# Optimization experiments

Measured on AMD Instinct MI355X. Metric: run time of the kernel, lower is better.

## Reference

```python
import jax, jax.numpy as jnp
import numpy as np

SIZES = {"a": 1024, "b": 512, "c": 2048}
OUT = 1024
N_STREAMS = 3
EPS = 1e-5


def _layer_norm(x, w, b):
    mu = jnp.mean(x, axis=-1, keepdims=True)
    var = jnp.mean(jnp.square(x - mu), axis=-1, keepdims=True)
    return (x - mu) * jax.lax.rsqrt(var + EPS) * w + b


def setup_inputs() -> dict:
    key = jax.random.key(0)
    ks = iter(jax.random.split(key, 32))
    B = 32768
    inp = {}
    for name, d in SIZES.items():
        inp[f"x_{name}"] = jax.random.normal(next(ks), (B, d), dtype=jnp.float32)
        inp[f"ln_w_{name}"] = jnp.ones((d,), dtype=jnp.float32)
        inp[f"ln_b_{name}"] = jnp.zeros((d,), dtype=jnp.float32)
        inp[f"W_{name}"] = jax.random.normal(next(ks), (d, OUT), dtype=jnp.float32) / np.sqrt(d)
        inp[f"b_{name}"] = jnp.zeros((OUT,), dtype=jnp.float32)
        # gating linear: size -> n_streams * gate_size (gate_size = OUT, pointwise)
        inp[f"Wg_{name}"] = 0.005 * jax.random.normal(next(ks), (d, N_STREAMS * OUT), dtype=jnp.float32)
        inp[f"bg_{name}"] = jnp.zeros((N_STREAMS * OUT,), dtype=jnp.float32)
    return inp


def reference(x_a, ln_w_a, ln_b_a, W_a, b_a, Wg_a, bg_a,
              x_b, ln_w_b, ln_b_b, W_b, b_b, Wg_b, bg_b,
              x_c, ln_w_c, ln_b_c, W_c, b_c, Wg_c, bg_c):
    xs = [x_a, x_b, x_c]
    lns = [(ln_w_a, ln_b_a), (ln_w_b, ln_b_b), (ln_w_c, ln_b_c)]
    lins = [(W_a, b_a), (W_b, b_b), (W_c, b_c)]
    gats = [(Wg_a, bg_a), (Wg_b, bg_b), (Wg_c, bg_c)]

    gate_logits = 0.0
    outputs = []
    for x, (lw, lb), (W, b), (Wg, bg) in zip(xs, lns, lins, gats):
        f = jax.nn.relu(_layer_norm(x, lw, lb))          # [B, d]
        outputs.append(f @ W + b)                         # [B, OUT]
        gate_logits = gate_logits + (f @ Wg + bg)         # [B, 3*OUT]

    B = x_a.shape[0]
    gate = jax.nn.softmax(gate_logits.reshape(B, N_STREAMS, OUT), axis=1)  # [B,3,OUT]
    out = sum(gate[:, i] * outputs[i] for i in range(N_STREAMS))
    return out
```

## Files before the change

kernel.cpp:

```cpp
#include <hip/hip_runtime.h>
#include <hip/hip_bf16.h>
#include <stdint.h>

#define B_ROWS 32768
#define KTOT   3584
#define NC     6144
#define OUT_N  1024

typedef unsigned short ushort_t;
typedef __attribute__((ext_vector_type(8))) short bf16x8;
typedef __attribute__((ext_vector_type(4))) float f32x4;

__device__ __forceinline__ float b2f(unsigned short u) {
    union { unsigned int i; float f; } x; x.i = ((unsigned int)u) << 16; return x.f;
}
__device__ __forceinline__ unsigned short f2b(float f) {
    union { float f; unsigned int i; } x; x.f = f;
    unsigned int r = x.i + 0x7fffu + ((x.i >> 16) & 1u);
    return (unsigned short)(r >> 16);
}

__device__ __forceinline__ void gload_lds16(const void* g, void* l) {
    auto g1 = reinterpret_cast<const __attribute__((address_space(1))) char*>(
        reinterpret_cast<uintptr_t>(g));
    auto l3 = reinterpret_cast<__attribute__((address_space(3))) char*>(
        (uint32_t)reinterpret_cast<uintptr_t>(l));
    __builtin_amdgcn_global_load_lds(g1, l3, 16, 0, 0);
}

__global__ __launch_bounds__(256) void pack_wt_kernel(
    const float* __restrict__ Wa, const float* __restrict__ Wga,
    const float* __restrict__ Wb, const float* __restrict__ Wgb,
    const float* __restrict__ Wc, const float* __restrict__ Wgc,
    ushort_t* __restrict__ WT)
{
    int s = blockIdx.y;
    const float *Ws, *Wgs; int d, koff;
    if (s == 0)      { Ws = Wa; Wgs = Wga; d = 1024; koff = 0;    }
    else if (s == 1) { Ws = Wb; Wgs = Wgb; d = 512;  koff = 1024; }
    else             { Ws = Wc; Wgs = Wgc; d = 2048; koff = 1536; }
    int kt = blockIdx.x >> 6;
    int ntile = blockIdx.x & 63;
    if (kt >= (d >> 6)) return;
    int k0 = kt * 64, n0 = ntile * 64;
    const float* src; int ld, ncol0;
    if (n0 < 1024) { src = Ws;  ld = 1024; ncol0 = n0; }
    else           { src = Wgs; ld = 3072; ncol0 = n0 - 1024; }

    __shared__ float tile[64][65];
    int tx = threadIdx.x & 63, ty = threadIdx.x >> 6;
    for (int r = ty; r < 64; r += 4)
        tile[r][tx] = src[(size_t)(k0 + r) * ld + ncol0 + tx];
    __syncthreads();
    for (int r = ty; r < 64; r += 4)
        WT[(size_t)(n0 + r) * KTOT + koff + k0 + tx] = f2b(tile[tx][r]);
}

__global__ __launch_bounds__(256) void pack_bias_kernel(
    const float* __restrict__ ba, const float* __restrict__ bb, const float* __restrict__ bc,
    const float* __restrict__ bga, const float* __restrict__ bgb, const float* __restrict__ bgc,
    float* __restrict__ bias)
{
    int i = blockIdx.x * 256 + threadIdx.x;
    if (i >= NC) return;
    float v;
    if (i < 1024)      v = ba[i];
    else if (i < 2048) v = bb[i - 1024];
    else if (i < 3072) v = bc[i - 2048];
    else { int g = i - 3072; v = bga[g] + bgb[g] + bgc[g]; }
    bias[i] = v;
}

__global__ __launch_bounds__(256) void ln_relu_kernel(
    const float* __restrict__ xa, const float* __restrict__ xb, const float* __restrict__ xc,
    const float* __restrict__ wa, const float* __restrict__ wb, const float* __restrict__ wc,
    const float* __restrict__ ba, const float* __restrict__ bb, const float* __restrict__ bc,
    ushort_t* __restrict__ F)
{
    int row = blockIdx.x;
    int s = blockIdx.y;
    const float *x, *w, *b; int d, koff;
    if (s == 0)      { x = xa; w = wa; b = ba; d = 1024; koff = 0;    }
    else if (s == 1) { x = xb; w = wb; b = bb; d = 512;  koff = 1024; }
    else             { x = xc; w = wc; b = bc; d = 2048; koff = 1536; }
    const float* xr = x + (size_t)row * d;
    int tid = threadIdx.x;

    float s1 = 0.f, s2 = 0.f;
    for (int i = tid * 4; i < d; i += 1024) {
        float4 v = *(const float4*)(xr + i);
        s1 += v.x + v.y + v.z + v.w;
        s2 += v.x * v.x + v.y * v.y + v.z * v.z + v.w * v.w;
    }
    for (int o = 32; o > 0; o >>= 1) {
        s1 += __shfl_down(s1, o, 64);
        s2 += __shfl_down(s2, o, 64);
    }
    __shared__ float red1[4], red2[4], bcast[2];
    int wv = tid >> 6, ln = tid & 63;
    if (ln == 0) { red1[wv] = s1; red2[wv] = s2; }
    __syncthreads();
    if (tid == 0) {
        float t1 = red1[0] + red1[1] + red1[2] + red1[3];
        float t2 = red2[0] + red2[1] + red2[2] + red2[3];
        float mean = t1 / d;
        float var = t2 / d - mean * mean;
        bcast[0] = mean;
        bcast[1] = rsqrtf(var + 1e-5f);
    }
    __syncthreads();
    float mean = bcast[0], rstd = bcast[1];

    ushort_t* Fr = F + (size_t)row * KTOT + koff;
    for (int i = tid * 4; i < d; i += 1024) {
        float4 v  = *(const float4*)(xr + i);
        float4 wv4 = *(const float4*)(w + i);
        float4 bv4 = *(const float4*)(b + i);
        float o0 = fmaxf(0.f, (v.x - mean) * rstd * wv4.x + bv4.x);
        float o1 = fmaxf(0.f, (v.y - mean) * rstd * wv4.y + bv4.y);
        float o2 = fmaxf(0.f, (v.z - mean) * rstd * wv4.z + bv4.z);
        float o3 = fmaxf(0.f, (v.w - mean) * rstd * wv4.w + bv4.w);
        union { ushort_t u[4]; uint2 v2; } pk;
        pk.u[0] = f2b(o0); pk.u[1] = f2b(o1); pk.u[2] = f2b(o2); pk.u[3] = f2b(o3);
        *(uint2*)(Fr + i) = pk.v2;
    }
}

__global__ __launch_bounds__(512, 2) void gemm_kernel(
    const ushort_t* __restrict__ F, const ushort_t* __restrict__ WT,
    const float* __restrict__ bias, ushort_t* __restrict__ C)
{
    extern __shared__ ushort_t lds_u16[];
    char* lds = (char*)lds_u16;

    int bid = blockIdx.x;
    int newid = (bid & 7) * 384 + (bid >> 3);
    int rowpanel = newid / 24;
    int j = newid % 24;
    int row0 = rowpanel * 256;
    int n0, koff, klen, c0;
    if (j < 4)       { n0 = j * 256;            koff = 0;    klen = 1024; c0 = j * 256; }
    else if (j < 8)  { n0 = (j - 4) * 256;      koff = 1024; klen = 512;  c0 = 1024 + (j - 4) * 256; }
    else if (j < 12) { n0 = (j - 8) * 256;      koff = 1536; klen = 2048; c0 = 2048 + (j - 8) * 256; }
    else             { n0 = 1024 + (j - 12) * 256; koff = 0; klen = 3584; c0 = 3072 + (j - 12) * 256; }

    int tid = threadIdx.x, w = tid >> 6, l = tid & 63;
    int wm0 = (w >> 2) * 128;
    int wn0 = (w & 3) * 64;

    int srow = w * 32 + (l >> 3);
    int scol = (((l & 7) ^ (l >> 3)) << 3);
    const ushort_t* Ag = F  + (size_t)(row0 + srow) * KTOT + koff + scol;
    const ushort_t* Bg = WT + (size_t)(n0   + srow) * KTOT + koff + scol;
    char* ldsAw = lds + (size_t)w * 4096;

#define STAGE(bufsel, kt) do {                                              \
        const ushort_t* ag_ = Ag + (kt) * 64;                               \
        const ushort_t* bg_ = Bg + (kt) * 64;                               \
        char* la_ = ldsAw + (bufsel) * 65536;                               \
        _Pragma("unroll")                                                   \
        for (int jj = 0; jj < 4; ++jj) {                                    \
            gload_lds16(ag_ + jj * 8 * KTOT, la_ + jj * 1024);              \
            gload_lds16(bg_ + jj * 8 * KTOT, la_ + 32768 + jj * 1024);      \
        }                                                                   \
    } while (0)

    int rl = l & 15;
    int c16_0 = ((l >> 4)    ) ^ (l & 7);
    int c16_1 = ((l >> 4) + 4) ^ (l & 7);
    int aoff0 = (wm0 + rl) * 128 + c16_0 * 16;
    int aoff1 = (wm0 + rl) * 128 + c16_1 * 16;
    int boff0 = 32768 + (wn0 + rl) * 128 + c16_0 * 16;
    int boff1 = 32768 + (wn0 + rl) * 128 + c16_1 * 16;

    f32x4 acc[8][4];
    #pragma unroll
    for (int mi = 0; mi < 8; ++mi)
        #pragma unroll
        for (int ni = 0; ni < 4; ++ni)
            acc[mi][ni] = (f32x4){0.f, 0.f, 0.f, 0.f};

    int nkt = klen >> 6;

    STAGE(0, 0);
    STAGE(1, 1);

#define TILE_BODY(CUR, VMCNT_ASM, DO_STAGE, TNEXT)                          \
    {                                                                       \
        asm volatile(VMCNT_ASM ::: "memory");                               \
        __builtin_amdgcn_s_barrier();                                       \
        const char* Ab_ = lds + (CUR) * 65536;                              \
        bf16x8 a0[8], a1[8], b0[4], b1[4];                                  \
        _Pragma("unroll")                                                   \
        for (int mi = 0; mi < 8; ++mi)                                      \
            a0[mi] = *(const bf16x8*)(Ab_ + aoff0 + mi * 2048);             \
        _Pragma("unroll")                                                   \
        for (int ni = 0; ni < 4; ++ni)                                      \
            b0[ni] = *(const bf16x8*)(Ab_ + boff0 + ni * 2048);             \
        _Pragma("unroll")                                                   \
        for (int mi = 0; mi < 8; ++mi)                                      \
            a1[mi] = *(const bf16x8*)(Ab_ + aoff1 + mi * 2048);             \
        _Pragma("unroll")                                                   \
        for (int ni = 0; ni < 4; ++ni)                                      \
            b1[ni] = *(const bf16x8*)(Ab_ + boff1 + ni * 2048);             \
        __builtin_amdgcn_s_setprio(1);                                      \
        _Pragma("unroll")                                                   \
        for (int mi = 0; mi < 8; ++mi)                                      \
            _Pragma("unroll")                                               \
            for (int ni = 0; ni < 4; ++ni)                                  \
                acc[mi][ni] = __builtin_amdgcn_mfma_f32_16x16x32_bf16(      \
                    a0[mi], b0[ni], acc[mi][ni], 0, 0, 0);                  \
        __builtin_amdgcn_s_setprio(0);                                      \
        asm volatile("s_waitcnt lgkmcnt(0)" ::: "memory");                  \
        __builtin_amdgcn_s_barrier();                                       \
        if (DO_STAGE) STAGE(CUR, TNEXT);                                    \
        __builtin_amdgcn_s_setprio(1);                                      \
        _Pragma("unroll")                                                   \
        for (int mi = 0; mi < 8; ++mi)                                      \
            _Pragma("unroll")                                               \
            for (int ni = 0; ni < 4; ++ni)                                  \
                acc[mi][ni] = __builtin_amdgcn_mfma_f32_16x16x32_bf16(      \
                    a1[mi], b1[ni], acc[mi][ni], 0, 0, 0);                  \
        __builtin_amdgcn_s_setprio(0);                                      \
    }

    for (int t = 0; t < nkt - 1; ++t) {
        int cur = t & 1;
        TILE_BODY(cur, "s_waitcnt vmcnt(8)", (t + 2 < nkt), t + 2)
    }
    {
        int cur = (nkt - 1) & 1;
        TILE_BODY(cur, "s_waitcnt vmcnt(0)", false, 0)
    }
#undef TILE_BODY
#undef STAGE

    #pragma unroll
    for (int ni = 0; ni < 4; ++ni) {
        int col = c0 + wn0 + ni * 16 + rl;
        float bv = bias[col];
        #pragma unroll
        for (int mi = 0; mi < 8; ++mi) {
            int rbase = row0 + wm0 + mi * 16 + (l >> 4) * 4;
            #pragma unroll
            for (int r = 0; r < 4; ++r)
                C[(size_t)(rbase + r) * NC + col] = f2b(acc[mi][ni][r] + bv);
        }
    }
}

typedef __attribute__((ext_vector_type(8))) unsigned short u16x8;

__global__ __launch_bounds__(256) void fuse_kernel(
    const ushort_t* __restrict__ C, float* __restrict__ out)
{
    int t = blockIdx.x * 256 + threadIdx.x;
    int b  = t >> 7;
    int j0 = (t & 127) << 3;
    const ushort_t* Cr = C + (size_t)b * NC;
    u16x8 oa = *(const u16x8*)(Cr + j0);
    u16x8 ob = *(const u16x8*)(Cr + 1024 + j0);
    u16x8 oc = *(const u16x8*)(Cr + 2048 + j0);
    u16x8 g0 = *(const u16x8*)(Cr + 3072 + j0);
    u16x8 g1 = *(const u16x8*)(Cr + 4096 + j0);
    u16x8 g2 = *(const u16x8*)(Cr + 5120 + j0);
    float res[8];
    #pragma unroll
    for (int k = 0; k < 8; ++k) {
        float a0 = b2f(g0[k]), a1 = b2f(g1[k]), a2 = b2f(g2[k]);
        float m = fmaxf(a0, fmaxf(a1, a2));
        float e0 = __expf(a0 - m), e1 = __expf(a1 - m), e2 = __expf(a2 - m);
        float inv = 1.f / (e0 + e1 + e2);
        res[k] = (e0 * b2f(oa[k]) + e1 * b2f(ob[k]) + e2 * b2f(oc[k])) * inv;
    }
    float* op = out + (size_t)b * 1024 + j0;
    *(float4*)op       = (float4){res[0], res[1], res[2], res[3]};
    *(float4*)(op + 4) = (float4){res[4], res[5], res[6], res[7]};
}

extern "C" void kernel_launch(void* const* d_in, const int* in_sizes, int n_in,
                              void* d_out, int out_size, void* d_ws, size_t ws_size,
                              hipStream_t stream)
{
    const float* x_a   = (const float*)d_in[0];
    const float* lnw_a = (const float*)d_in[1];
    const float* lnb_a = (const float*)d_in[2];
    const float* W_a   = (const float*)d_in[3];
    const float* b_a   = (const float*)d_in[4];
    const float* Wg_a  = (const float*)d_in[5];
    const float* bg_a  = (const float*)d_in[6];
    const float* x_b   = (const float*)d_in[7];
    const float* lnw_b = (const float*)d_in[8];
    const float* lnb_b = (const float*)d_in[9];
    const float* W_b   = (const float*)d_in[10];
    const float* b_b   = (const float*)d_in[11];
    const float* Wg_b  = (const float*)d_in[12];
    const float* bg_b  = (const float*)d_in[13];
    const float* x_c   = (const float*)d_in[14];
    const float* lnw_c = (const float*)d_in[15];
    const float* lnb_c = (const float*)d_in[16];
    const float* W_c   = (const float*)d_in[17];
    const float* b_c   = (const float*)d_in[18];
    const float* Wg_c  = (const float*)d_in[19];
    const float* bg_c  = (const float*)d_in[20];

    char* ws = (char*)d_ws;
    ushort_t* F    = (ushort_t*)ws;
    ushort_t* WT   = (ushort_t*)(ws + 234881024);
    ushort_t* Cbuf = (ushort_t*)(ws + 234881024 + 29360128);
    float*    bias = (float*)   (ws + 234881024 + 29360128 + 402653184);

    hipLaunchKernelGGL(pack_wt_kernel, dim3(2048, 3), dim3(256), 0, stream,
                       W_a, Wg_a, W_b, Wg_b, W_c, Wg_c, WT);
    hipLaunchKernelGGL(pack_bias_kernel, dim3(24), dim3(256), 0, stream,
                       b_a, b_b, b_c, bg_a, bg_b, bg_c, bias);
    hipLaunchKernelGGL(ln_relu_kernel, dim3(32768, 3), dim3(256), 0, stream,
                       x_a, x_b, x_c, lnw_a, lnw_b, lnw_c, lnb_a, lnb_b, lnb_c, F);
    hipLaunchKernelGGL(gemm_kernel, dim3(3072), dim3(512), 131072, stream,
                       F, WT, bias, Cbuf);
    hipLaunchKernelGGL(fuse_kernel, dim3(16384), dim3(256), 0, stream,
                       Cbuf, (float*)d_out);
}
```

Before: 1.099 ms.

## Restructure GEMM main loop into four interleaved quadrant phases with staggered loads

Splits each K-tile of the bf16 GEMM into four MFMA quadrants. LDS reads and global-to-LDS staging for the next tiles are interleaved between them, so memory traffic overlaps compute at a finer grain. LDS reads use inline-asm ds_read_b128 with immediate offsets, and sched_barriers pin the order. The cost is more s_barriers per tile, and the loop clamps tail tile indices, so redundant loads are issued at the end.

```diff
diff --git a/kernel.cpp b/kernel.cpp
--- a/kernel.cpp
+++ b/kernel.cpp
@@ -26,6 +26,13 @@
     auto l3 = reinterpret_cast<__attribute__((address_space(3))) char*>(
         (uint32_t)reinterpret_cast<uintptr_t>(l));
     __builtin_amdgcn_global_load_lds(g1, l3, 16, 0, 0);
+}
+
+template<int OFF>
+__device__ __forceinline__ bf16x8 dsr(uint32_t addr) {
+    bf16x8 d;
+    asm volatile("ds_read_b128 %0, %1 offset:%2" : "=v"(d) : "v"(addr), "i"(OFF));
+    return d;
 }
 
 __global__ __launch_bounds__(256) void pack_wt_kernel(
@@ -131,7 +138,6 @@
     const float* __restrict__ bias, ushort_t* __restrict__ C)
 {
     extern __shared__ ushort_t lds_u16[];
-    char* lds = (char*)lds_u16;
 
     int bid = blockIdx.x;
     int newid = (bid & 7) * 384 + (bid >> 3);
@@ -152,26 +158,52 @@
     int scol = (((l & 7) ^ (l >> 3)) << 3);
     const ushort_t* Ag = F  + (size_t)(row0 + srow) * KTOT + koff + scol;
     const ushort_t* Bg = WT + (size_t)(n0   + srow) * KTOT + koff + scol;
-    char* ldsAw = lds + (size_t)w * 4096;
-
-#define STAGE(bufsel, kt) do {                                              \
-        const ushort_t* ag_ = Ag + (kt) * 64;                               \
-        const ushort_t* bg_ = Bg + (kt) * 64;                               \
-        char* la_ = ldsAw + (bufsel) * 65536;                               \
-        _Pragma("unroll")                                                   \
-        for (int jj = 0; jj < 4; ++jj) {                                    \
-            gload_lds16(ag_ + jj * 8 * KTOT, la_ + jj * 1024);              \
-            gload_lds16(bg_ + jj * 8 * KTOT, la_ + 32768 + jj * 1024);      \
-        }                                                                   \
-    } while (0)
+
+    uint32_t lds_base = (uint32_t)(uintptr_t)lds_u16;
+    uint32_t ldsStA = lds_base + (uint32_t)w * 4096u;
+
+#define STG_A(SELOFF, kt, JJ0) do {                                              \
+        gload_lds16(Ag + (size_t)(kt) * 64 + (size_t)(JJ0) * 8 * KTOT,           \
+                    (void*)(uintptr_t)(ldsStA + (SELOFF) + (JJ0) * 1024u));      \
+        gload_lds16(Ag + (size_t)(kt) * 64 + (size_t)((JJ0) + 1) * 8 * KTOT,     \
+                    (void*)(uintptr_t)(ldsStA + (SELOFF) + ((JJ0) + 1) * 1024u)); } while (0)
+#define STG_B(SELOFF, kt, JJ0) do {                                              \
+        gload_lds16(Bg + (size_t)(kt) * 64 + (size_t)(JJ0) * 8 * KTOT,           \
+                    (void*)(uintptr_t)(ldsStA + 32768u + (SELOFF) + (JJ0) * 1024u)); \
+        gload_lds16(Bg + (size_t)(kt) * 64 + (size_t)((JJ0) + 1) * 8 * KTOT,     \
+                    (void*)(uintptr_t)(ldsStA + 32768u + (SELOFF) + ((JJ0) + 1) * 1024u)); } while (0)
 
     int rl = l & 15;
     int c16_0 = ((l >> 4)    ) ^ (l & 7);
     int c16_1 = ((l >> 4) + 4) ^ (l & 7);
-    int aoff0 = (wm0 + rl) * 128 + c16_0 * 16;
-    int aoff1 = (wm0 + rl) * 128 + c16_1 * 16;
-    int boff0 = 32768 + (wn0 + rl) * 128 + c16_0 * 16;
-    int boff1 = 32768 + (wn0 + rl) * 128 + c16_1 * 16;
+    uint32_t aA0 = lds_base + (uint32_t)((wm0 + rl) * 128 + c16_0 * 16);
+    uint32_t aA1 = lds_base + (uint32_t)((wm0 + rl) * 128 + c16_1 * 16);
+    uint32_t aB0 = lds_base + 32768u + (uint32_t)((wn0 + rl) * 128 + c16_0 * 16);
+    uint32_t aB1 = lds_base + 32768u + (uint32_t)((wn0 + rl) * 128 + c16_1 * 16);
+
+#define R_A4(dst, base, MI0) do {                          \
+        dst[0] = dsr<((MI0)+0)*2048>(base);                \
+        dst[1] = dsr<((MI0)+1)*2048>(base);                \
+        dst[2] = dsr<((MI0)+2)*2048>(base);                \
+        dst[3] = dsr<((MI0)+3)*2048>(base); } while (0)
+#define R_B2(dst, base, NI0) do {                          \
+        dst[0] = dsr<((NI0)+0)*2048>(base);                \
+        dst[1] = dsr<((NI0)+1)*2048>(base); } while (0)
+
+#define MFMA_Q(Aks0, Aks1, Bks0, Bks1, MI0, NI0) do {                            \
+        _Pragma("unroll")                                                        \
+        for (int mi = 0; mi < 4; ++mi)                                           \
+            _Pragma("unroll")                                                    \
+            for (int ni = 0; ni < 2; ++ni)                                       \
+                acc[(MI0)+mi][(NI0)+ni] = __builtin_amdgcn_mfma_f32_16x16x32_bf16( \
+                    Aks0[mi], Bks0[ni], acc[(MI0)+mi][(NI0)+ni], 0, 0, 0);       \
+        _Pragma("unroll")                                                        \
+        for (int mi = 0; mi < 4; ++mi)                                           \
+            _Pragma("unroll")                                                    \
+            for (int ni = 0; ni < 2; ++ni)                                       \
+                acc[(MI0)+mi][(NI0)+ni] = __builtin_amdgcn_mfma_f32_16x16x32_bf16( \
+                    Aks1[mi], Bks1[ni], acc[(MI0)+mi][(NI0)+ni], 0, 0, 0);       \
+        } while (0)
 
     f32x4 acc[8][4];
     #pragma unroll
@@ -182,58 +214,64 @@
 
     int nkt = klen >> 6;
 
-    STAGE(0, 0);
-    STAGE(1, 1);
-
-#define TILE_BODY(CUR, VMCNT_ASM, DO_STAGE, TNEXT)                          \
-    {                                                                       \
-        asm volatile(VMCNT_ASM ::: "memory");                               \
-        __builtin_amdgcn_s_barrier();                                       \
-        const char* Ab_ = lds + (CUR) * 65536;                              \
-        bf16x8 a0[8], a1[8], b0[4], b1[4];                                  \
-        _Pragma("unroll")                                                   \
-        for (int mi = 0; mi < 8; ++mi)                                      \
-            a0[mi] = *(const bf16x8*)(Ab_ + aoff0 + mi * 2048);             \
-        _Pragma("unroll")                                                   \
-        for (int ni = 0; ni < 4; ++ni)                                      \
-            b0[ni] = *(const bf16x8*)(Ab_ + boff0 + ni * 2048);             \
-        _Pragma("unroll")                                                   \
-        for (int mi = 0; mi < 8; ++mi)                                      \
-            a1[mi] = *(const bf16x8*)(Ab_ + aoff1 + mi * 2048);             \
-        _Pragma("unroll")                                                   \
-        for (int ni = 0; ni < 4; ++ni)                                      \
-            b1[ni] = *(const bf16x8*)(Ab_ + boff1 + ni * 2048);             \
-        __builtin_amdgcn_s_setprio(1);                                      \
-        _Pragma("unroll")                                                   \
-        for (int mi = 0; mi < 8; ++mi)                                      \
-            _Pragma("unroll")                                               \
-            for (int ni = 0; ni < 4; ++ni)                                  \
-                acc[mi][ni] = __builtin_amdgcn_mfma_f32_16x16x32_bf16(      \
-                    a0[mi], b0[ni], acc[mi][ni], 0, 0, 0);                  \
-        __builtin_amdgcn_s_setprio(0);                                      \
-        asm volatile("s_waitcnt lgkmcnt(0)" ::: "memory");                  \
-        __builtin_amdgcn_s_barrier();                                       \
-        if (DO_STAGE) STAGE(CUR, TNEXT);                                    \
-        __builtin_amdgcn_s_setprio(1);                                      \
-        _Pragma("unroll")                                                   \
-        for (int mi = 0; mi < 8; ++mi)                                      \
-            _Pragma("unroll")                                               \
-            for (int ni = 0; ni < 4; ++ni)                                  \
-                acc[mi][ni] = __builtin_amdgcn_mfma_f32_16x16x32_bf16(      \
-                    a1[mi], b1[ni], acc[mi][ni], 0, 0, 0);                  \
-        __builtin_amdgcn_s_setprio(0);                                      \
-    }
-
-    for (int t = 0; t < nkt - 1; ++t) {
-        int cur = t & 1;
-        TILE_BODY(cur, "s_waitcnt vmcnt(8)", (t + 2 < nkt), t + 2)
-    }
-    {
-        int cur = (nkt - 1) & 1;
-        TILE_BODY(cur, "s_waitcnt vmcnt(0)", false, 0)
-    }
-#undef TILE_BODY
-#undef STAGE
+    STG_A(0u, 0, 0); STG_A(0u, 0, 2); STG_B(0u, 0, 0); STG_B(0u, 0, 2);
+    STG_A(65536u, 1, 0);
+
+    for (int t = 0; t < nkt; ++t) {
+        const uint32_t co  = (t & 1) ? 65536u : 0u;
+        const uint32_t no_ = co ^ 65536u;
+        int t1 = (t + 1 < nkt) ? t + 1 : nkt - 1;
+        int t2 = (t + 2 < nkt) ? t + 2 : nkt - 1;
+
+        asm volatile("s_waitcnt vmcnt(2)" ::: "memory");
+        __builtin_amdgcn_s_barrier();
+
+        bf16x8 alo0[4], alo1[4], ahi0[4], ahi1[4];
+        bf16x8 blo0[2], blo1[2], bhi0[2], bhi1[2];
+
+        R_A4(alo0, aA0 + co, 0); R_A4(alo1, aA1 + co, 0);
+        R_B2(blo0, aB0 + co, 0); R_B2(blo1, aB1 + co, 0);
+        STG_A(no_, t1, 2);
+        __builtin_amdgcn_s_barrier();
+        asm volatile("s_waitcnt lgkmcnt(0)" ::: "memory");
+        __builtin_amdgcn_sched_barrier(0);
+        __builtin_amdgcn_s_setprio(1);
+        MFMA_Q(alo0, alo1, blo0, blo1, 0, 0);
+        __builtin_amdgcn_s_setprio(0);
+        __builtin_amdgcn_s_barrier();
+
+        R_B2(bhi0, aB0 + co, 2); R_B2(bhi1, aB1 + co, 2);
+        STG_B(no_, t1, 0);
+        __builtin_amdgcn_s_barrier();
+        asm volatile("s_waitcnt lgkmcnt(0)" ::: "memory");
+        __builtin_amdgcn_sched_barrier(0);
+        __builtin_amdgcn_s_setprio(1);
+        MFMA_Q(alo0, alo1, bhi0, bhi1, 0, 2);
+        __builtin_amdgcn_s_setprio(0);
+        __builtin_amdgcn_s_barrier();
+
+        R_A4(ahi0, aA0 + co, 4); R_A4(ahi1, aA1 + co, 4);
+        STG_B(no_, t1, 2);
+        __builtin_amdgcn_s_barrier();
+        asm volatile("s_waitcnt lgkmcnt(0)" ::: "memory");
+        __builtin_amdgcn_sched_barrier(0);
+        __builtin_amdgcn_s_setprio(1);
+        MFMA_Q(ahi0, ahi1, blo0, blo1, 4, 0);
+        __builtin_amdgcn_s_setprio(0);
+        __builtin_amdgcn_s_barrier();
+
+        STG_A(co, t2, 0);
+        __builtin_amdgcn_s_barrier();
+        __builtin_amdgcn_s_setprio(1);
+        MFMA_Q(ahi0, ahi1, bhi0, bhi1, 4, 2);
+        __builtin_amdgcn_s_setprio(0);
+    }
+
+#undef STG_A
+#undef STG_B
+#undef R_A4
+#undef R_B2
+#undef MFMA_Q
 
     #pragma unroll
     for (int ni = 0; ni < 4; ++ni) {
```

Result: no change. 1.081 ms (-1.7%).
